# Performance work log

Hardware: AMD Instinct MI355X
Metric: run time of the kernel (lower is better)

Reference implementation:

```python
import jax, jax.numpy as jnp
import numpy as np

HID = 64        # HID_DIM of seq2seq encoder
NL = 2          # N_LAYERS
D = HID * NL    # dim_hidden = 128
TYPES = 16      # node op types; Input=0, Const=1
MAX_ET = 32     # max edge_type id
NUM_ROUNDS = 2


def _gru_cell(x, h, Wih, Whh, bih, bhh):
    # torch GRU gate ordering: r, z, n
    gi = x @ Wih.T + bih
    gh = h @ Whh.T + bhh
    ir, iz, inn = jnp.split(gi, 3, axis=-1)
    hr, hz, hn = jnp.split(gh, 3, axis=-1)
    r = jax.nn.sigmoid(ir + hr)
    z = jax.nn.sigmoid(iz + hz)
    n = jnp.tanh(inn + r * hn)
    return (1.0 - z) * n + z * h


def _posenc(n, d):
    pos = jnp.arange(n, dtype=jnp.float32)[:, None]
    i = jnp.arange(d // 2, dtype=jnp.float32)[None, :]
    inv = jnp.exp(-jnp.log(10000.0) * (2.0 * i / d))
    pe = jnp.zeros((n, d), jnp.float32)
    pe = pe.at[:, 0::2].set(jnp.sin(pos * inv))
    pe = pe.at[:, 1::2].set(jnp.cos(pos * inv))
    return pe


def _forward(x, edge_index, edge_type, sim_res, seq_len,
             enc_Wih0, enc_Whh0, enc_bih0, enc_bhh0,
             enc_Wih1, enc_Whh1, enc_bih1, enc_bhh1,
             Wq, Wk, Wv, op_emb, mlp_W1, mlp_b1, mlp_W2, mlp_b2,
             gru_Wih, gru_Whh, gru_bih, gru_bhh):
    N = x.shape[0]
    # --- seq2seq encode (2-layer GRU over time), computed for all nodes then masked ---
    xs = jnp.swapaxes(sim_res[:, :seq_len, :], 0, 1)  # [T, N, W]
    h0 = jnp.zeros((N, HID), sim_res.dtype)
    h1 = jnp.zeros((N, HID), sim_res.dtype)

    def step(carry, xt):
        h0, h1 = carry
        h0 = _gru_cell(xt, h0, enc_Wih0, enc_Whh0, enc_bih0, enc_bhh0)
        h1 = _gru_cell(h0, h1, enc_Wih1, enc_Whh1, enc_bih1, enc_bhh1)
        return (h0, h1), None

    (h0, h1), _ = jax.lax.scan(step, (h0, h1), xs)
    enc = jnp.concatenate([h0, h1], axis=-1)  # [N, D] = permute(1,0,2).flatten(1)
    mask = (x[:, 0] == 1) | (x[:, 1] == 1)    # Input | Const nodes
    node_emb = jnp.where(mask[:, None], enc, 0.0)

    src, dst = edge_index[0], edge_index[1]
    edge_op = jnp.argmax(x[dst], axis=1)       # [E]
    pe = _posenc(MAX_ET, D)
    edge_feat = pe[edge_type] + op_emb[edge_op]  # [E, D]
    scale = 1.0 / jnp.sqrt(jnp.float32(D))

    for _ in range(NUM_ROUNDS):
        kf = node_emb[src] + edge_feat         # [E, D]
        q = node_emb[dst] @ Wq.T
        k = kf @ Wk.T
        v = kf @ Wv.T
        score = jnp.sum(q * k, axis=-1) * scale  # [E]
        m = jax.ops.segment_max(score, dst, num_segments=N)
        ex = jnp.exp(score - m[dst])
        den = jax.ops.segment_sum(ex, dst, num_segments=N)
        alpha = ex / (den[dst] + 1e-9)
        aggr = jax.ops.segment_sum(alpha[:, None] * v, dst, num_segments=N)  # [N, D]
        aggr = jax.nn.relu(aggr @ mlp_W1.T + mlp_b1) @ mlp_W2.T + mlp_b2
        node_emb = _gru_cell(aggr, node_emb, gru_Wih, gru_Whh, gru_bih, gru_bhh)
    return node_emb


def setup_inputs() -> dict:
    key = jax.random.key(0)
    ks = jax.random.split(key, 24)
    N, E, T, W = 20000, 320000, 32, 32
    s = 0.05

    def g(k, shape):
        return jax.random.normal(k, shape, dtype=jnp.float32) * s

    node_type = jax.random.randint(ks[0], (N,), 0, TYPES)
    x = jax.nn.one_hot(node_type, TYPES, dtype=jnp.float32)
    edge_index = jax.random.randint(ks[1], (2, E), 0, N)
    edge_type = jax.random.randint(ks[2], (E,), 0, MAX_ET)
    sim_res = jax.random.uniform(ks[3], (N, T, W), dtype=jnp.float32)
    return {
        "x": x, "edge_index": edge_index, "edge_type": edge_type,
        "sim_res": sim_res, "seq_len": 32,
        "enc_Wih0": g(ks[4], (3 * HID, W)), "enc_Whh0": g(ks[5], (3 * HID, HID)),
        "enc_bih0": g(ks[6], (3 * HID,)), "enc_bhh0": g(ks[7], (3 * HID,)),
        "enc_Wih1": g(ks[8], (3 * HID, HID)), "enc_Whh1": g(ks[9], (3 * HID, HID)),
        "enc_bih1": g(ks[10], (3 * HID,)), "enc_bhh1": g(ks[11], (3 * HID,)),
        "Wq": g(ks[12], (D, D)), "Wk": g(ks[13], (D, D)), "Wv": g(ks[14], (D, D)),
        "op_emb": g(ks[15], (TYPES, D)),
        "mlp_W1": g(ks[16], (D, D)), "mlp_b1": g(ks[17], (D,)),
        "mlp_W2": g(ks[18], (D, D)), "mlp_b2": g(ks[19], (D,)),
        "gru_Wih": g(ks[20], (3 * D, D)), "gru_Whh": g(ks[21], (3 * D, D)),
        "gru_bih": g(ks[22], (3 * D,)), "gru_bhh": g(ks[23], (3 * D,)),
    }


def reference(x, edge_index, edge_type, sim_res, seq_len,
              enc_Wih0, enc_Whh0, enc_bih0, enc_bhh0,
              enc_Wih1, enc_Whh1, enc_bih1, enc_bhh1,
              Wq, Wk, Wv, op_emb, mlp_W1, mlp_b1, mlp_W2, mlp_b2,
              gru_Wih, gru_Whh, gru_bih, gru_bhh):
    return _forward(x, edge_index, edge_type, sim_res, seq_len,
                    enc_Wih0, enc_Whh0, enc_bih0, enc_bhh0,
                    enc_Wih1, enc_Whh1, enc_bih1, enc_bhh1,
                    Wq, Wk, Wv, op_emb, mlp_W1, mlp_b1, mlp_W2, mlp_b2,
                    gru_Wih, gru_Whh, gru_bih, gru_bhh)
```

## Files before the change

kernel.cpp:

```cpp
#include <hip/hip_runtime.h>

typedef unsigned int uint;
typedef unsigned short ushort;

typedef __attribute__((ext_vector_type(8))) short bf8;
typedef __attribute__((ext_vector_type(4))) float f32x4;
typedef _Float16 half_t;
typedef __attribute__((ext_vector_type(8))) half_t h8;

__device__ __forceinline__ ushort f2bf(float f){
  uint u = __builtin_bit_cast(uint, f);
  u = u + 0x7FFFu + ((u >> 16) & 1u);
  return (ushort)(u >> 16);
}
__device__ __forceinline__ float bfl(uint u){ return __builtin_bit_cast(float, u << 16); }
__device__ __forceinline__ float bfh(uint u){ return __builtin_bit_cast(float, u & 0xFFFF0000u); }
__device__ __forceinline__ uint pkhalf(float a, float b){
  ushort lo = __builtin_bit_cast(ushort, (half_t)a);
  ushort hi = __builtin_bit_cast(ushort, (half_t)b);
  return (uint)lo | ((uint)hi << 16);
}
__device__ __forceinline__ float sigmoidf_(float x){ return 1.0f/(1.0f + __expf(-x)); }
__device__ __forceinline__ float tanhf_(float x){
  x = fminf(15.0f, fmaxf(-15.0f, x));
  float t = __expf(-2.0f*x);
  return (1.0f - t)/(1.0f + t);
}
__device__ __forceinline__ f32x4 mfma_f16(h8 a, h8 b, f32x4 c){
  return __builtin_amdgcn_mfma_f32_16x16x32_f16(a, b, c, 0, 0, 0);
}
__device__ __forceinline__ h8 ldw8(const float* p){
  f32x4 a = *(const f32x4*)p, b = *(const f32x4*)(p+4);
  h8 v;
  #pragma unroll
  for (int j=0;j<4;j++){ v[j] = (half_t)a[j]; v[4+j] = (half_t)b[j]; }
  return v;
}

__global__ __launch_bounds__(256) void k_prep(const float* __restrict__ x,
    const int* __restrict__ dst,
    int* __restrict__ typ, int* __restrict__ mlist, int* __restrict__ cnt,
    int* __restrict__ deg, float* __restrict__ Hf, ushort* __restrict__ Hb,
    int N, int E){
  int i = blockIdx.x*256 + threadIdx.x;
  int total = gridDim.x*256;
  if (i < N){
    const float* xr = x + (size_t)i*16;
    int t = 0;
    #pragma unroll
    for (int j=0;j<16;j++) if (xr[j] > 0.5f) t = j;
    typ[i] = t;
    if (t < 2){
      int p = atomicAdd(cnt, 1);
      mlist[p] = i;
    }
  }
  if (i < E) atomicAdd(&deg[dst[i]], 1);
  f32x4 z4 = (f32x4)0.0f;
  for (int j = i; j < N*32; j += total) ((f32x4*)Hf)[j] = z4;
  uint2 z2; z2.x = 0u; z2.y = 0u;
  for (int j = i; j < N*32; j += total) ((uint2*)Hb)[j] = z2;
}

__global__ __launch_bounds__(256) void k_cvt(
    const float* wq, const float* wk, const float* wv,
    const float* w1, const float* w2, const float* wih, const float* whh,
    const float* __restrict__ op_emb,
    ushort* oqkv, ushort* o1, ushort* o2, ushort* oih, ushort* ohh,
    ushort* __restrict__ EF){
  int i = blockIdx.x*256 + threadIdx.x;
  int stride = gridDim.x*256;
  for (int j=i; j<16384; j+=stride){
    oqkv[j]       = f2bf(wq[j]);
    oqkv[16384+j] = f2bf(wk[j]);
    oqkv[32768+j] = f2bf(wv[j]);
    o1[j] = f2bf(w1[j]);
    o2[j] = f2bf(w2[j]);
  }
  for (int j=i; j<49152; j+=stride){ oih[j]=f2bf(wih[j]); ohh[j]=f2bf(whh[j]); }
  for (int idx=i; idx<512*128; idx+=stride){
    int r = idx >> 7, d = idx & 127;
    int et = r >> 4, op = r & 15;
    int j = d >> 1;
    float inv = __expf(-0.1439115683f * (float)j);
    float ang = (float)et * inv;
    float v = (d & 1) ? __cosf(ang) : __sinf(ang);
    EF[idx] = f2bf(v + op_emb[op*128 + d]);
  }
}

template<int RELU, int HASBIAS>
__global__ __launch_bounds__(256) void k_gemm(
    const ushort* __restrict__ A, const ushort* __restrict__ B,
    const float* __restrict__ bias, ushort* __restrict__ C, int M, int N){
  int lane = threadIdx.x & 63, wv = threadIdx.x >> 6;
  int tM = blockIdx.x*64 + (wv>>1)*32;
  int tN = blockIdx.y*64 + (wv&1)*32;
  int r16 = lane & 15, kg = (lane>>4)*8;
  f32x4 acc[2][2];
  #pragma unroll
  for (int i=0;i<2;i++)
    #pragma unroll
    for (int j=0;j<2;j++) acc[i][j] = (f32x4)0.0f;
  for (int k0=0;k0<128;k0+=32){
    bf8 a[2], b[2];
    #pragma unroll
    for (int i=0;i<2;i++){
      int row = tM + i*16 + r16; if (row > M-1) row = M-1;
      a[i] = *(const bf8*)(A + (size_t)row*128 + k0 + kg);
    }
    #pragma unroll
    for (int j=0;j<2;j++){
      int col = tN + j*16 + r16;
      b[j] = *(const bf8*)(B + (size_t)col*128 + k0 + kg);
    }
    #pragma unroll
    for (int i=0;i<2;i++)
      #pragma unroll
      for (int j=0;j<2;j++)
        acc[i][j] = __builtin_amdgcn_mfma_f32_16x16x32_bf16(a[i], b[j], acc[i][j], 0, 0, 0);
  }
  #pragma unroll
  for (int i=0;i<2;i++)
    #pragma unroll
    for (int j=0;j<2;j++){
      int col = tN + j*16 + r16;
      float bs = HASBIAS ? bias[col] : 0.0f;
      #pragma unroll
      for (int q=0;q<4;q++){
        int row = tM + i*16 + (lane>>4)*4 + q;
        if (row < M){
          float v = acc[i][j][q] + bs;
          if (RELU) v = fmaxf(v, 0.0f);
          C[(size_t)row*N + col] = f2bf(v);
        }
      }
    }
}

__global__ __launch_bounds__(512, 1) void k_enc4(
    const float* __restrict__ sim_res, const int* __restrict__ seqlen,
    const float* __restrict__ Wih0, const float* __restrict__ Whh0,
    const float* __restrict__ bih0, const float* __restrict__ bhh0,
    const float* __restrict__ Wih1, const float* __restrict__ Whh1,
    const float* __restrict__ bih1, const float* __restrict__ bhh1,
    const int* __restrict__ mlist, const int* __restrict__ cntp,
    float* __restrict__ Hf, ushort* __restrict__ Hb){
  int C = *cntp;
  int base = blockIdx.x * 16;
  if (C == 0 || base >= C) return;
  int tid = threadIdx.x;
  int w = tid >> 6, l = tid & 63;
  int node = l & 15, hi = l >> 4;
  int grp = w >> 2;
  int ws  = w & 3;

  __shared__ int nod[16];
  __shared__ __align__(16) float  Xs[16*32*32];
  __shared__ __align__(16) ushort H0h[2][16*64], H1h[2][16*64];

  if (tid < 16){
    int idx = base + tid;
    nod[tid] = mlist[idx < C ? idx : C-1];
  }
  for (int i = tid; i < 16*64; i += 512){
    H0h[0][i] = 0; H0h[1][i] = 0; H1h[0][i] = 0; H1h[1][i] = 0;
  }
  __syncthreads();

  for (int m = tid; m < 4096; m += 512){
    int nm = m >> 8, tt = (m >> 3) & 31, c = m & 7;
    int cs = c ^ (nm & 7);
    f32x4 v = *(const f32x4*)(sim_res + (size_t)nod[nm]*1024 + tt*32 + cs*4);
    *(f32x4*)(Xs + m*4) = v;
  }

  int rr = 16*ws + node;
  h8 zf;
  #pragma unroll
  for (int j=0;j<8;j++) zf[j] = (half_t)0.f;
  h8 Ai_r[2] = {zf, zf}, Ai_z[2] = {zf, zf}, Ai_n[2] = {zf, zf};
  h8 Ah_r[2], Ah_z[2], Ah_n[2];
  if (grp == 0){
    Ai_r[0] = ldw8(Wih0 + (size_t)rr*32        + hi*8);
    Ai_z[0] = ldw8(Wih0 + (size_t)(64+rr)*32   + hi*8);
    Ai_n[0] = ldw8(Wih0 + (size_t)(128+rr)*32  + hi*8);
    #pragma unroll
    for (int s=0;s<2;s++){
      Ah_r[s] = ldw8(Whh0 + (size_t)rr*64       + s*32 + hi*8);
      Ah_z[s] = ldw8(Whh0 + (size_t)(64+rr)*64  + s*32 + hi*8);
      Ah_n[s] = ldw8(Whh0 + (size_t)(128+rr)*64 + s*32 + hi*8);
    }
  } else {
    #pragma unroll
    for (int s=0;s<2;s++){
      Ai_r[s] = ldw8(Wih1 + (size_t)rr*64       + s*32 + hi*8);
      Ai_z[s] = ldw8(Wih1 + (size_t)(64+rr)*64  + s*32 + hi*8);
      Ai_n[s] = ldw8(Wih1 + (size_t)(128+rr)*64 + s*32 + hi*8);
      Ah_r[s] = ldw8(Whh1 + (size_t)rr*64       + s*32 + hi*8);
      Ah_z[s] = ldw8(Whh1 + (size_t)(64+rr)*64  + s*32 + hi*8);
      Ah_n[s] = ldw8(Whh1 + (size_t)(128+rr)*64 + s*32 + hi*8);
    }
  }
  const float* bi = grp ? bih1 : bih0;
  const float* bh = grp ? bhh1 : bhh0;
  float br[4], bz[4], bni[4], bnh[4];
  #pragma unroll
  for (int q=0;q<4;q++){
    int row = 16*ws + hi*4 + q;
    br[q]  = bi[row]      + bh[row];
    bz[q]  = bi[64+row]   + bh[64+row];
    bni[q] = bi[128+row];
    bnh[q] = bh[128+row];
  }

  int T = *seqlen; if (T > 32) T = 32; if (T < 0) T = 0;
  float hm[4] = {0.f, 0.f, 0.f, 0.f};

  const int swz = (node & 7) << 4;
  const int wo  = node * 128;
  const int wba = 32*ws + 8*hi;
  const int rd0 = wo + ((16*hi) ^ swz);
  const int rd1 = wo + ((64 + 16*hi) ^ swz);
  const int xc0 = (2*hi)   ^ (node & 7);
  const int xc1 = (2*hi+1) ^ (node & 7);
  const float* xrow = Xs + node*1024;

  __syncthreads();

  for (int k = 0; k <= T; ++k){
    int cur = k & 1;
    bool act = grp ? (k >= 1) : (k < T);
    if (act){
      h8 in0 = zf, in1 = zf, st0, st1;
      if (grp == 0){
        f32x4 xa = *(const f32x4*)(xrow + k*32 + xc0*4);
        f32x4 xb = *(const f32x4*)(xrow + k*32 + xc1*4);
        #pragma unroll
        for (int j=0;j<4;j++){ in0[j] = (half_t)xa[j]; in0[4+j] = (half_t)xb[j]; }
        st0 = *(const h8*)((const char*)H0h[cur] + rd0);
        st1 = *(const h8*)((const char*)H0h[cur] + rd1);
      } else {
        in0 = *(const h8*)((const char*)H0h[cur] + rd0);
        in1 = *(const h8*)((const char*)H0h[cur] + rd1);
        st0 = *(const h8*)((const char*)H1h[cur] + rd0);
        st1 = *(const h8*)((const char*)H1h[cur] + rd1);
      }
      f32x4 ar = {br[0],br[1],br[2],br[3]};
      f32x4 az = {bz[0],bz[1],bz[2],bz[3]};
      f32x4 an = {bni[0],bni[1],bni[2],bni[3]};
      f32x4 hn = {bnh[0],bnh[1],bnh[2],bnh[3]};
      ar = mfma_f16(Ai_r[0], in0, ar);
      az = mfma_f16(Ai_z[0], in0, az);
      an = mfma_f16(Ai_n[0], in0, an);
      if (grp){
        ar = mfma_f16(Ai_r[1], in1, ar);
        az = mfma_f16(Ai_z[1], in1, az);
        an = mfma_f16(Ai_n[1], in1, an);
      }
      ar = mfma_f16(Ah_r[0], st0, ar); ar = mfma_f16(Ah_r[1], st1, ar);
      az = mfma_f16(Ah_z[0], st0, az); az = mfma_f16(Ah_z[1], st1, az);
      hn = mfma_f16(Ah_n[0], st0, hn); hn = mfma_f16(Ah_n[1], st1, hn);
      #pragma unroll
      for (int q=0;q<4;q++){
        float r = sigmoidf_(ar[q]);
        float z = sigmoidf_(az[q]);
        float n = tanhf_(an[q] + r*hn[q]);
        hm[q] = (1.f - z)*n + z*hm[q];
      }
      char* outb = grp ? (char*)H1h[cur^1] : (char*)H0h[cur^1];
      *(uint*)(outb + wo + ( wba      ^ swz)) = pkhalf(hm[0], hm[1]);
      *(uint*)(outb + wo + ((wba + 4) ^ swz)) = pkhalf(hm[2], hm[3]);
    }
    __syncthreads();
  }

  if (base + node < C){
    int nd = nod[node];
    int off = grp ? 64 : 0;
    #pragma unroll
    for (int q=0;q<4;q++){
      int j = off + 16*ws + hi*4 + q;
      Hf[(size_t)nd*128 + j] = hm[q];
      Hb[(size_t)nd*128 + j] = f2bf(hm[q]);
    }
  }
}

__global__ __launch_bounds__(1024) void k_scan(const int* __restrict__ deg,
    int* __restrict__ rowptr, int* __restrict__ cursor, int N){
  __shared__ int wsum[16];
  __shared__ int carry_s;
  int tid = threadIdx.x, lane = tid & 63, wid = tid >> 6;
  if (tid == 0) carry_s = 0;
  __syncthreads();
  int nch = (N + 1023) / 1024;
  for (int c=0; c<nch; ++c){
    int i = c*1024 + tid;
    int v = (i < N) ? deg[i] : 0;
    int x = v;
    #pragma unroll
    for (int off=1; off<64; off<<=1){
      int t = __shfl_up(x, off, 64);
      if (lane >= off) x += t;
    }
    if (lane == 63) wsum[wid] = x;
    __syncthreads();
    int base = carry_s;
    int woff = 0;
    for (int w2=0; w2<wid; ++w2) woff += wsum[w2];
    int excl = base + woff + x - v;
    if (i < N){ rowptr[i] = excl; cursor[i] = excl; }
    __syncthreads();
    if (tid == 0){
      int s = 0;
      for (int w2=0; w2<16; ++w2) s += wsum[w2];
      carry_s = base + s;
    }
    __syncthreads();
  }
  if (tid == 0) rowptr[N] = carry_s;
}

__global__ __launch_bounds__(256) void k_scatter(const int* __restrict__ src,
    const int* __restrict__ dst, const int* __restrict__ etype, const int* __restrict__ typ,
    int* __restrict__ cursor, int* __restrict__ es_src, int* __restrict__ es_tab, int E){
  int e = blockIdx.x*256 + threadIdx.x;
  if (e < E){
    int d = dst[e];
    int pos = atomicAdd(&cursor[d], 1);
    es_src[pos] = src[e];
    es_tab[pos] = etype[e]*16 + typ[d];
  }
}

__global__ __launch_bounds__(256) void k_attn(
    const uint* __restrict__ QKV, const uint* __restrict__ KVT,
    const int* __restrict__ rowptr, const int* __restrict__ es_src, const int* __restrict__ es_tab,
    uint* __restrict__ aggr, int N){
  int w = threadIdx.x >> 6, lane = threadIdx.x & 63;
  int dst = blockIdx.x*4 + w;
  if (dst >= N) return;
  uint qu = QKV[(size_t)dst*192 + lane];
  const float scale = 0.08838834764831845f;
  float q0 = bfl(qu)*scale, q1 = bfh(qu)*scale;
  int s0 = rowptr[dst], s1 = rowptr[dst+1];
  float m = -1e30f, den = 0.f, a0 = 0.f, a1 = 0.f;
  int p = s0;
  for (; p + 2 <= s1; p += 2){
    int srcA = es_src[p],   tbA = es_tab[p];
    int srcB = es_src[p+1], tbB = es_tab[p+1];
    uint kuA = QKV[(size_t)srcA*192 + 64 + lane],  ktA = KVT[(size_t)tbA*128 + lane];
    uint vuA = QKV[(size_t)srcA*192 + 128 + lane], vtA = KVT[(size_t)tbA*128 + 64 + lane];
    uint kuB = QKV[(size_t)srcB*192 + 64 + lane],  ktB = KVT[(size_t)tbB*128 + lane];
    uint vuB = QKV[(size_t)srcB*192 + 128 + lane], vtB = KVT[(size_t)tbB*128 + 64 + lane];
    float sA = q0*(bfl(kuA)+bfl(ktA)) + q1*(bfh(kuA)+bfh(ktA));
    float sB = q0*(bfl(kuB)+bfl(ktB)) + q1*(bfh(kuB)+bfh(ktB));
    #pragma unroll
    for (int off=32; off; off>>=1){
      sA += __shfl_xor(sA, off);
      sB += __shfl_xor(sB, off);
    }
    float nm = fmaxf(m, fmaxf(sA, sB));
    float c  = __expf(m - nm);
    float pA = __expf(sA - nm), pB = __expf(sB - nm);
    den = den*c + pA + pB;
    a0  = a0*c + pA*(bfl(vuA)+bfl(vtA)) + pB*(bfl(vuB)+bfl(vtB));
    a1  = a1*c + pA*(bfh(vuA)+bfh(vtA)) + pB*(bfh(vuB)+bfh(vtB));
    m = nm;
  }
  for (; p < s1; ++p){
    int src = es_src[p], tb = es_tab[p];
    uint ku = QKV[(size_t)src*192 + 64 + lane],  kt = KVT[(size_t)tb*128 + lane];
    uint vu = QKV[(size_t)src*192 + 128 + lane], vt = KVT[(size_t)tb*128 + 64 + lane];
    float s = q0*(bfl(ku)+bfl(kt)) + q1*(bfh(ku)+bfh(kt));
    #pragma unroll
    for (int off=32; off; off>>=1) s += __shfl_xor(s, off);
    float nm = fmaxf(m, s);
    float c  = __expf(m - nm);
    float pw = __expf(s - nm);
    den = den*c + pw;
    a0  = a0*c + pw*(bfl(vu)+bfl(vt));
    a1  = a1*c + pw*(bfh(vu)+bfh(vt));
    m = nm;
  }
  float inv = 1.0f/(den + 1e-9f);
  a0 *= inv; a1 *= inv;
  aggr[(size_t)dst*64 + lane] = ((uint)f2bf(a1) << 16) | (uint)f2bf(a0);
}

__global__ __launch_bounds__(256) void k_gru(
    const ushort* __restrict__ Xb, const ushort* Hbf,
    const ushort* __restrict__ Wih, const ushort* __restrict__ Whh,
    const float* __restrict__ bih, const float* __restrict__ bhh,
    const float* Hf_in, float* Hf_out, ushort* Hb_out, int M){
  int lane = threadIdx.x & 63, wv = threadIdx.x >> 6;
  int nb = blockIdx.x * 32;
  int r16 = lane & 15, kg = (lane>>4)*8;
  f32x4 gi[2][6], gh[2][6];
  #pragma unroll
  for (int i=0;i<2;i++)
    #pragma unroll
    for (int c=0;c<6;c++){ gi[i][c] = (f32x4)0.0f; gh[i][c] = (f32x4)0.0f; }
  int cts[6] = {2*wv, 2*wv+1, 2*wv+8, 2*wv+9, 2*wv+16, 2*wv+17};
  for (int k0=0;k0<128;k0+=32){
    bf8 ax[2], ah[2];
    #pragma unroll
    for (int i=0;i<2;i++){
      int row = nb + i*16 + r16; if (row > M-1) row = M-1;
      ax[i] = *(const bf8*)(Xb  + (size_t)row*128 + k0 + kg);
      ah[i] = *(const bf8*)(Hbf + (size_t)row*128 + k0 + kg);
    }
    #pragma unroll
    for (int c=0;c<6;c++){
      bf8 bi = *(const bf8*)(Wih + (size_t)(cts[c]*16 + r16)*128 + k0 + kg);
      bf8 bh = *(const bf8*)(Whh + (size_t)(cts[c]*16 + r16)*128 + k0 + kg);
      #pragma unroll
      for (int i=0;i<2;i++){
        gi[i][c] = __builtin_amdgcn_mfma_f32_16x16x32_bf16(ax[i], bi, gi[i][c], 0, 0, 0);
        gh[i][c] = __builtin_amdgcn_mfma_f32_16x16x32_bf16(ah[i], bh, gh[i][c], 0, 0, 0);
      }
    }
  }
  __syncthreads();
  #pragma unroll
  for (int i=0;i<2;i++)
    #pragma unroll
    for (int p=0;p<2;p++){
      int jcol = (2*wv + p)*16 + r16;
      float bir = bih[jcol], biz = bih[128+jcol], bin = bih[256+jcol];
      float bhr = bhh[jcol], bhz = bhh[128+jcol], bhn = bhh[256+jcol];
      #pragma unroll
      for (int q=0;q<4;q++){
        int node = nb + i*16 + (lane>>4)*4 + q;
        if (node < M){
          float gr  = gi[i][p][q]   + bir + gh[i][p][q]   + bhr;
          float gz  = gi[i][2+p][q] + biz + gh[i][2+p][q] + bhz;
          float inn = gi[i][4+p][q] + bin;
          float hnn = gh[i][4+p][q] + bhn;
          float rr = sigmoidf_(gr), zz = sigmoidf_(gz);
          float nn = tanhf_(inn + rr*hnn);
          float h = Hf_in[(size_t)node*128 + jcol];
          float o = (1.f - zz)*nn + zz*h;
          Hf_out[(size_t)node*128 + jcol] = o;
          Hb_out[(size_t)node*128 + jcol] = f2bf(o);
        }
      }
    }
}

extern "C" void kernel_launch(void* const* d_in, const int* in_sizes, int n_in,
                              void* d_out, int out_size, void* d_ws, size_t ws_size,
                              hipStream_t stream){
  const float* x       = (const float*)d_in[0];
  const int*   ei      = (const int*)d_in[1];
  const int*   etype   = (const int*)d_in[2];
  const float* sim_res = (const float*)d_in[3];
  const int*   seqlen  = (const int*)d_in[4];
  const float* eWih0 = (const float*)d_in[5];
  const float* eWhh0 = (const float*)d_in[6];
  const float* ebih0 = (const float*)d_in[7];
  const float* ebhh0 = (const float*)d_in[8];
  const float* eWih1 = (const float*)d_in[9];
  const float* eWhh1 = (const float*)d_in[10];
  const float* ebih1 = (const float*)d_in[11];
  const float* ebhh1 = (const float*)d_in[12];
  const float* Wq = (const float*)d_in[13];
  const float* Wk = (const float*)d_in[14];
  const float* Wv = (const float*)d_in[15];
  const float* op_emb = (const float*)d_in[16];
  const float* W1 = (const float*)d_in[17];
  const float* b1 = (const float*)d_in[18];
  const float* W2 = (const float*)d_in[19];
  const float* b2 = (const float*)d_in[20];
  const float* gWih = (const float*)d_in[21];
  const float* gWhh = (const float*)d_in[22];
  const float* gbih = (const float*)d_in[23];
  const float* gbhh = (const float*)d_in[24];

  const int N = in_sizes[0] / 16;
  const int E = in_sizes[2];

  char* p = (char*)d_ws;
  auto take = [&](size_t b)->void*{ void* r = (void*)p; p += (b + 255) & ~(size_t)255; return r; };

  float*  Hf    = (float*) take((size_t)N*128*4);
  ushort* Hb    = (ushort*)take((size_t)N*128*2);
  ushort* QKV   = (ushort*)take((size_t)N*384*2);
  ushort* Ag    = (ushort*)take((size_t)N*128*2);
  ushort* T1    = (ushort*)take((size_t)N*128*2);
  ushort* Xin   = (ushort*)take((size_t)N*128*2);
  ushort* EF    = (ushort*)take((size_t)512*128*2);
  ushort* KVtab = (ushort*)take((size_t)512*256*2);
  ushort* wqkv  = (ushort*)take((size_t)3*16384*2);
  ushort* w1_b  = (ushort*)take((size_t)16384*2);
  ushort* w2_b  = (ushort*)take((size_t)16384*2);
  ushort* wih_b = (ushort*)take((size_t)49152*2);
  ushort* whh_b = (ushort*)take((size_t)49152*2);
  int* typ    = (int*)take((size_t)N*4);
  int* mlist  = (int*)take((size_t)N*4);
  int* cnt    = (int*)take(256);
  int* deg    = (int*)take((size_t)N*4);
  int* rowptr = (int*)take((size_t)(N+1)*4);
  int* cursor = (int*)take((size_t)N*4);
  int* es_src = (int*)take((size_t)E*4);
  int* es_tab = (int*)take((size_t)E*4);

  hipMemsetAsync(cnt, 0, 4, stream);
  hipMemsetAsync(deg, 0, (size_t)N*4, stream);

  int gE = (E + 255) / 256;
  k_prep<<<gE, 256, 0, stream>>>(x, ei + E, typ, mlist, cnt, deg, Hf, Hb, N, E);
  k_cvt<<<256, 256, 0, stream>>>(Wq, Wk, Wv, W1, W2, gWih, gWhh, op_emb,
                                 wqkv, w1_b, w2_b, wih_b, whh_b, EF);
  k_gemm<0,0><<<dim3(8,4), 256, 0, stream>>>(EF, wqkv + 16384, nullptr, KVtab, 512, 256);
  k_enc4<<<(N+15)/16, 512, 0, stream>>>(sim_res, seqlen, eWih0, eWhh0, ebih0, ebhh0,
                                        eWih1, eWhh1, ebih1, ebhh1, mlist, cnt, Hf, Hb);
  k_scan<<<1, 1024, 0, stream>>>(deg, rowptr, cursor, N);
  k_scatter<<<gE, 256, 0, stream>>>(ei, ei + E, etype, typ, cursor, es_src, es_tab, E);

  dim3 gq((N+63)/64, 6);
  dim3 g1((N+63)/64, 2);
  for (int r=0; r<2; ++r){
    k_gemm<0,0><<<gq, 256, 0, stream>>>(Hb, wqkv, nullptr, QKV, N, 384);
    k_attn<<<(N+3)/4, 256, 0, stream>>>((const uint*)QKV, (const uint*)KVtab,
                                        rowptr, es_src, es_tab, (uint*)Ag, N);
    k_gemm<1,1><<<g1, 256, 0, stream>>>(Ag, w1_b, b1, T1, N, 128);
    k_gemm<0,1><<<g1, 256, 0, stream>>>(T1, w2_b, b2, Xin, N, 128);
    float* hf_out = (r == 1) ? (float*)d_out : Hf;
    k_gru<<<(N+31)/32, 256, 0, stream>>>(Xin, Hb, wih_b, whh_b, gbih, gbhh,
                                         Hf, hf_out, Hb, N);
  }
}
```

Measured before the change: 341.0 us.

## Fuse MLP GEMMs and GRU update into one kernel via LDS staging

The two MLP GEMMs (ReLU then linear) and the GRU cell are merged into a single kernel per 32-node tile, with intermediates held in an XOR-swizzled shared-memory buffer instead of global T1/Xin arrays. The GRU r and z gate accumulations now sum input and hidden contributions into one accumulator, which cuts accumulator registers. This removes two launches per round and the global round trips of the intermediates. The cost is more work per block and a shared-memory footprint, and the weight reads are less amortized with 32-row tiles. The GEMM k-loop is also fully unrolled.

```diff
diff --git a/kernel.cpp b/kernel.cpp
--- a/kernel.cpp
+++ b/kernel.cpp
@@ -28,6 +28,9 @@
 }
 __device__ __forceinline__ f32x4 mfma_f16(h8 a, h8 b, f32x4 c){
   return __builtin_amdgcn_mfma_f32_16x16x32_f16(a, b, c, 0, 0, 0);
+}
+__device__ __forceinline__ f32x4 mfma_bf(bf8 a, bf8 b, f32x4 c){
+  return __builtin_amdgcn_mfma_f32_16x16x32_bf16(a, b, c, 0, 0, 0);
 }
 __device__ __forceinline__ h8 ldw8(const float* p){
   f32x4 a = *(const f32x4*)p, b = *(const f32x4*)(p+4);
@@ -102,6 +105,7 @@
   for (int i=0;i<2;i++)
     #pragma unroll
     for (int j=0;j<2;j++) acc[i][j] = (f32x4)0.0f;
+  #pragma unroll
   for (int k0=0;k0<128;k0+=32){
     bf8 a[2], b[2];
     #pragma unroll
@@ -389,36 +393,131 @@
   aggr[(size_t)dst*64 + lane] = ((uint)f2bf(a1) << 16) | (uint)f2bf(a0);
 }
 
-__global__ __launch_bounds__(256) void k_gru(
-    const ushort* __restrict__ Xb, const ushort* Hbf,
+__global__ __launch_bounds__(256) void k_fused(
+    const ushort* __restrict__ Ag,
+    const ushort* __restrict__ W1b, const float* __restrict__ b1,
+    const ushort* __restrict__ W2b, const float* __restrict__ b2,
     const ushort* __restrict__ Wih, const ushort* __restrict__ Whh,
     const float* __restrict__ bih, const float* __restrict__ bhh,
-    const float* Hf_in, float* Hf_out, ushort* Hb_out, int M){
+    const ushort* Hbf, const float* Hf_in,
+    float* Hf_out, ushort* Hb_out, int M){
   int lane = threadIdx.x & 63, wv = threadIdx.x >> 6;
   int nb = blockIdx.x * 32;
-  int r16 = lane & 15, kg = (lane>>4)*8;
-  f32x4 gi[2][6], gh[2][6];
+  int r16 = lane & 15, kq = lane >> 4;
+
+  __shared__ __align__(16) ushort T[32*128];
+
+  {
+    f32x4 acc[2][2];
+    #pragma unroll
+    for (int i=0;i<2;i++)
+      #pragma unroll
+      for (int j=0;j<2;j++) acc[i][j] = (f32x4)0.0f;
+    #pragma unroll
+    for (int ks=0; ks<4; ++ks){
+      bf8 a[2], b[2];
+      #pragma unroll
+      for (int i=0;i<2;i++){
+        int row = nb + i*16 + r16; if (row > M-1) row = M-1;
+        a[i] = *(const bf8*)(Ag + (size_t)row*128 + ks*32 + kq*8);
+      }
+      #pragma unroll
+      for (int j=0;j<2;j++)
+        b[j] = *(const bf8*)(W1b + (size_t)(wv*32 + j*16 + r16)*128 + ks*32 + kq*8);
+      #pragma unroll
+      for (int i=0;i<2;i++)
+        #pragma unroll
+        for (int j=0;j<2;j++) acc[i][j] = mfma_bf(a[i], b[j], acc[i][j]);
+    }
+    #pragma unroll
+    for (int i=0;i<2;i++)
+      #pragma unroll
+      for (int j=0;j<2;j++){
+        int col = wv*32 + j*16 + r16;
+        float bs = b1[col];
+        #pragma unroll
+        for (int q=0;q<4;q++){
+          int row = i*16 + kq*4 + q;
+          float v = fmaxf(acc[i][j][q] + bs, 0.0f);
+          *(ushort*)((char*)T + ((row*256 + col*2) ^ ((row&7)<<4))) = f2bf(v);
+        }
+      }
+  }
+  __syncthreads();
+
+  {
+    f32x4 acc[2][2];
+    #pragma unroll
+    for (int i=0;i<2;i++)
+      #pragma unroll
+      for (int j=0;j<2;j++) acc[i][j] = (f32x4)0.0f;
+    #pragma unroll
+    for (int ks=0; ks<4; ++ks){
+      bf8 a[2], b[2];
+      #pragma unroll
+      for (int i=0;i<2;i++){
+        int row = i*16 + r16;
+        a[i] = *(const bf8*)((const char*)T + row*256 + ((ks*64 + kq*16) ^ ((row&7)<<4)));
+      }
+      #pragma unroll
+      for (int j=0;j<2;j++)
+        b[j] = *(const bf8*)(W2b + (size_t)(wv*32 + j*16 + r16)*128 + ks*32 + kq*8);
+      #pragma unroll
+      for (int i=0;i<2;i++)
+        #pragma unroll
+        for (int j=0;j<2;j++) acc[i][j] = mfma_bf(a[i], b[j], acc[i][j]);
+    }
+    __syncthreads();
+    #pragma unroll
+    for (int i=0;i<2;i++)
+      #pragma unroll
+      for (int j=0;j<2;j++){
+        int col = wv*32 + j*16 + r16;
+        float bs = b2[col];
+        #pragma unroll
+        for (int q=0;q<4;q++){
+          int row = i*16 + kq*4 + q;
+          *(ushort*)((char*)T + ((row*256 + col*2) ^ ((row&7)<<4))) = f2bf(acc[i][j][q] + bs);
+        }
+      }
+  }
+  __syncthreads();
+
+  f32x4 ar[2][2], az[2][2], ani[2][2], anh[2][2];
   #pragma unroll
   for (int i=0;i<2;i++)
     #pragma unroll
-    for (int c=0;c<6;c++){ gi[i][c] = (f32x4)0.0f; gh[i][c] = (f32x4)0.0f; }
-  int cts[6] = {2*wv, 2*wv+1, 2*wv+8, 2*wv+9, 2*wv+16, 2*wv+17};
-  for (int k0=0;k0<128;k0+=32){
+    for (int p2=0;p2<2;p2++){
+      ar[i][p2] = (f32x4)0.0f; az[i][p2] = (f32x4)0.0f;
+      ani[i][p2] = (f32x4)0.0f; anh[i][p2] = (f32x4)0.0f;
+    }
+  #pragma unroll
+  for (int ks=0; ks<4; ++ks){
     bf8 ax[2], ah[2];
     #pragma unroll
     for (int i=0;i<2;i++){
-      int row = nb + i*16 + r16; if (row > M-1) row = M-1;
-      ax[i] = *(const bf8*)(Xb  + (size_t)row*128 + k0 + kg);
-      ah[i] = *(const bf8*)(Hbf + (size_t)row*128 + k0 + kg);
-    }
-    #pragma unroll
-    for (int c=0;c<6;c++){
-      bf8 bi = *(const bf8*)(Wih + (size_t)(cts[c]*16 + r16)*128 + k0 + kg);
-      bf8 bh = *(const bf8*)(Whh + (size_t)(cts[c]*16 + r16)*128 + k0 + kg);
+      int row = i*16 + r16;
+      ax[i] = *(const bf8*)((const char*)T + row*256 + ((ks*64 + kq*16) ^ ((row&7)<<4)));
+      int grow = nb + row; if (grow > M-1) grow = M-1;
+      ah[i] = *(const bf8*)(Hbf + (size_t)grow*128 + ks*32 + kq*8);
+    }
+    #pragma unroll
+    for (int p2=0;p2<2;p2++){
+      int cb = wv*32 + p2*16 + r16;
+      bf8 wri = *(const bf8*)(Wih + (size_t)cb*128        + ks*32 + kq*8);
+      bf8 wrh = *(const bf8*)(Whh + (size_t)cb*128        + ks*32 + kq*8);
+      bf8 wzi = *(const bf8*)(Wih + (size_t)(128+cb)*128  + ks*32 + kq*8);
+      bf8 wzh = *(const bf8*)(Whh + (size_t)(128+cb)*128  + ks*32 + kq*8);
+      bf8 wni = *(const bf8*)(Wih + (size_t)(256+cb)*128  + ks*32 + kq*8);
+      bf8 wnh = *(const bf8*)(Whh + (size_t)(256+cb)*128  + ks*32 + kq*8);
       #pragma unroll
       for (int i=0;i<2;i++){
-        gi[i][c] = __builtin_amdgcn_mfma_f32_16x16x32_bf16(ax[i], bi, gi[i][c], 0, 0, 0);
-        gh[i][c] = __builtin_amdgcn_mfma_f32_16x16x32_bf16(ah[i], bh, gh[i][c], 0, 0, 0);
+        ar[i][p2]  = mfma_bf(ax[i], wri, ar[i][p2]);
+        ar[i][p2]  = mfma_bf(ah[i], wrh, ar[i][p2]);
+        az[i][p2]  = mfma_bf(ax[i], wzi, az[i][p2]);
+        az[i][p2]  = mfma_bf(ah[i], wzh, az[i][p2]);
+        ani[i][p2] = mfma_bf(ax[i], wni, ani[i][p2]);
+        anh[i][p2] = mfma_bf(ah[i], wnh, anh[i][p2]);
       }
     }
   }
@@ -426,22 +525,21 @@
   #pragma unroll
   for (int i=0;i<2;i++)
     #pragma unroll
-    for (int p=0;p<2;p++){
-      int jcol = (2*wv + p)*16 + r16;
-      float bir = bih[jcol], biz = bih[128+jcol], bin = bih[256+jcol];
-      float bhr = bhh[jcol], bhz = bhh[128+jcol], bhn = bhh[256+jcol];
+    for (int p2=0;p2<2;p2++){
+      int jcol = wv*32 + p2*16 + r16;
+      float br_  = bih[jcol]     + bhh[jcol];
+      float bz_  = bih[128+jcol] + bhh[128+jcol];
+      float bni_ = bih[256+jcol];
+      float bnh_ = bhh[256+jcol];
       #pragma unroll
       for (int q=0;q<4;q++){
-        int node = nb + i*16 + (lane>>4)*4 + q;
+        int node = nb + i*16 + kq*4 + q;
         if (node < M){
-          float gr  = gi[i][p][q]   + bir + gh[i][p][q]   + bhr;
-          float gz  = gi[i][2+p][q] + biz + gh[i][2+p][q] + bhz;
-          float inn = gi[i][4+p][q] + bin;
-          float hnn = gh[i][4+p][q] + bhn;
-          float rr = sigmoidf_(gr), zz = sigmoidf_(gz);
-          float nn = tanhf_(inn + rr*hnn);
+          float r = sigmoidf_(ar[i][p2][q] + br_);
+          float z = sigmoidf_(az[i][p2][q] + bz_);
+          float n = tanhf_(ani[i][p2][q] + bni_ + r*(anh[i][p2][q] + bnh_));
           float h = Hf_in[(size_t)node*128 + jcol];
-          float o = (1.f - zz)*nn + zz*h;
+          float o = (1.f - z)*n + z*h;
           Hf_out[(size_t)node*128 + jcol] = o;
           Hb_out[(size_t)node*128 + jcol] = f2bf(o);
         }
@@ -488,8 +586,6 @@
   ushort* Hb    = (ushort*)take((size_t)N*128*2);
   ushort* QKV   = (ushort*)take((size_t)N*384*2);
   ushort* Ag    = (ushort*)take((size_t)N*128*2);
-  ushort* T1    = (ushort*)take((size_t)N*128*2);
-  ushort* Xin   = (ushort*)take((size_t)N*128*2);
   ushort* EF    = (ushort*)take((size_t)512*128*2);
   ushort* KVtab = (ushort*)take((size_t)512*256*2);
   ushort* wqkv  = (ushort*)take((size_t)3*16384*2);
@@ -520,15 +616,13 @@
   k_scatter<<<gE, 256, 0, stream>>>(ei, ei + E, etype, typ, cursor, es_src, es_tab, E);
 
   dim3 gq((N+63)/64, 6);
-  dim3 g1((N+63)/64, 2);
   for (int r=0; r<2; ++r){
     k_gemm<0,0><<<gq, 256, 0, stream>>>(Hb, wqkv, nullptr, QKV, N, 384);
     k_attn<<<(N+3)/4, 256, 0, stream>>>((const uint*)QKV, (const uint*)KVtab,
                                         rowptr, es_src, es_tab, (uint*)Ag, N);
-    k_gemm<1,1><<<g1, 256, 0, stream>>>(Ag, w1_b, b1, T1, N, 128);
-    k_gemm<0,1><<<g1, 256, 0, stream>>>(T1, w2_b, b2, Xin, N, 128);
     float* hf_out = (r == 1) ? (float*)d_out : Hf;
-    k_gru<<<(N+31)/32, 256, 0, stream>>>(Xin, Hb, wih_b, whh_b, gbih, gbhh,
-                                         Hf, hf_out, Hb, N);
-  }
-}
+    k_fused<<<(N+31)/32, 256, 0, stream>>>(Ag, w1_b, b1, w2_b, b2,
+                                           wih_b, whh_b, gbih, gbhh,
+                                           Hb, Hf, hf_out, Hb, N);
+  }
+}
```

After: 314.7 us. 1.08x faster.
